# Kernel optimization log

Hardware: AMD Instinct MI355X
Metric: run time of the kernel (lower is better)

## Reference

```python
import jax, jax.numpy as jnp
import numpy as np

D_MODEL = 1024
N_HEADS = 16
D_HEAD = D_MODEL // N_HEADS
D_FF = 4096
B, S = 4, 1024
EPS = 1e-12


def layer_norm(x, gamma, beta):
    # Faithful to the torch module: unbiased std (ddof=1) and division by (std + eps).
    mean = jnp.mean(x, axis=-1, keepdims=True)
    var = jnp.sum((x - mean) ** 2, axis=-1, keepdims=True) / (x.shape[-1] - 1)
    std = jnp.sqrt(var)
    return gamma * (x - mean) / (std + EPS) + beta


def setup_inputs() -> dict:
    key = jax.random.key(0)
    ks = jax.random.split(key, 10)
    sc = lambda fan_in: 1.0 / np.sqrt(fan_in)
    inp = {
        "x": jax.random.normal(ks[0], (B, S, D_MODEL), dtype=jnp.float32),
        "ln1_g": jnp.ones((D_MODEL,), jnp.float32),
        "ln1_b": jnp.zeros((D_MODEL,), jnp.float32),
        "wq": jax.random.normal(ks[1], (D_MODEL, D_MODEL), jnp.float32) * sc(D_MODEL),
        "bq": jnp.zeros((D_MODEL,), jnp.float32),
        "wk": jax.random.normal(ks[2], (D_MODEL, D_MODEL), jnp.float32) * sc(D_MODEL),
        "bk": jnp.zeros((D_MODEL,), jnp.float32),
        "wv": jax.random.normal(ks[3], (D_MODEL, D_MODEL), jnp.float32) * sc(D_MODEL),
        "bv": jnp.zeros((D_MODEL,), jnp.float32),
        "ln2_g": jnp.ones((D_MODEL,), jnp.float32),
        "ln2_b": jnp.zeros((D_MODEL,), jnp.float32),
        "w1": jax.random.normal(ks[4], (D_FF, D_MODEL), jnp.float32) * sc(D_MODEL),
        "b1": jnp.zeros((D_FF,), jnp.float32),
        "w2": jax.random.normal(ks[5], (D_MODEL, D_FF), jnp.float32) * sc(D_FF),
        "b2": jnp.zeros((D_MODEL,), jnp.float32),
    }
    return inp


def reference(x, ln1_g, ln1_b, wq, bq, wk, bk, wv, bv, ln2_g, ln2_b, w1, b1, w2, b2):
    Bsz, Sq, D = x.shape
    residual = x
    h = layer_norm(x, ln1_g, ln1_b)
    # QKV projections (no output projection in the original module)
    q = (h @ wq.T + bq).reshape(Bsz, Sq, N_HEADS, D_HEAD)
    k = (h @ wk.T + bk).reshape(Bsz, Sq, N_HEADS, D_HEAD)
    v = (h @ wv.T + bv).reshape(Bsz, Sq, N_HEADS, D_HEAD)
    scores = jnp.einsum("bqhd,bkhd->bhqk", q, k) / np.sqrt(D_HEAD)
    attn = jax.nn.softmax(scores, axis=-1)  # [B, H, S, S]
    ctx = jnp.einsum("bhqk,bkhd->bqhd", attn, v).reshape(Bsz, Sq, D)
    out = ctx + residual
    residual = out
    h2 = layer_norm(out, ln2_g, ln2_b)
    # 1x1 conv FFN == per-token MLP with ReLU (dropout inactive at eval)
    ff = jax.nn.relu(h2 @ w1.T + b1) @ w2.T + b2
    out = ff + residual
    # torch returns attn flattened head-major: [H*B, S, S]
    attn_ret = jnp.transpose(attn, (1, 0, 2, 3)).reshape(N_HEADS * Bsz, Sq, Sq)
    return out, attn_ret
```

## Files before the change

kernel.cpp:

```cpp
#include <hip/hip_runtime.h>
#include <cstdint>
#include <cstddef>

#define SEQ 1024
#define DM 1024
#define DF 4096
#define NH 16
#define DH 64
#define BSZ 4
#define NTOK (BSZ*SEQ)
#define QKVSZ ((long)NTOK*DM)

typedef short s16x8 __attribute__((ext_vector_type(8)));
typedef float f32x4 __attribute__((ext_vector_type(4)));

__device__ __forceinline__ unsigned short f2bf(float f) {
  union { float f; unsigned u; } c; c.f = f;
  unsigned u = c.u;
  return (unsigned short)((u + 0x7fffu + ((u >> 16) & 1u)) >> 16);
}
__device__ __forceinline__ float bf2f(unsigned short b) {
  union { unsigned u; float f; } c; c.u = ((unsigned)b) << 16; return c.f;
}

__device__ __forceinline__ void gll16(const void* g, void* l) {
  __builtin_amdgcn_global_load_lds(
      (__attribute__((address_space(1))) void*)(g),
      (__attribute__((address_space(3))) void*)(l), 16, 0, 0);
}

template<int BM, int BN, int WM, int WN, int EPI>
__launch_bounds__(256)
__global__ void gemm_k(const unsigned short* __restrict__ A,
                       const unsigned short* __restrict__ W,
                       const float* __restrict__ bias,
                       void* __restrict__ outp,
                       const float* __restrict__ resid,
                       int nB, int K, int aRow, int wRow, int oRow,
                       float scale) {
  constexpr int BK = 32;
  __shared__ unsigned short At[BM*BK];
  __shared__ unsigned short Wt[BN*BK];
  const int tid = threadIdx.x;
  const int mb = (int)blockIdx.x / nB, nb = (int)blockIdx.x % nB;
  const long aBase = (long)mb*BM*aRow;
  const long wBase = (long)nb*BN*wRow;
  const int wave = tid >> 6, lane = tid & 63;
  const int quad = lane >> 4, l16 = lane & 15;
  constexpr int WGN = BN / WN;
  const int wm = (wave / WGN) * WM, wn = (wave % WGN) * WN;
  constexpr int MT = WM/16, NT = WN/16;
  f32x4 acc[MT][NT] = {};
  const int srow = tid >> 2, skof = (tid & 3) * 8;

  for (int k0 = 0; k0 < K; k0 += BK) {
#pragma unroll
    for (int r = 0; r < BM; r += 64)
      gll16(A + aBase + (long)(r + srow)*aRow + k0 + skof, &At[(r + srow)*BK + skof]);
#pragma unroll
    for (int r = 0; r < BN; r += 64)
      gll16(W + wBase + (long)(r + srow)*wRow + k0 + skof, &Wt[(r + srow)*BK + skof]);
    __syncthreads();
    s16x8 af[MT];
#pragma unroll
    for (int mt = 0; mt < MT; ++mt)
      af[mt] = *(const s16x8*)&At[(wm + mt*16 + l16)*BK + quad*8];
#pragma unroll
    for (int nt = 0; nt < NT; ++nt) {
      s16x8 bfr = *(const s16x8*)&Wt[(wn + nt*16 + l16)*BK + quad*8];
#pragma unroll
      for (int mt = 0; mt < MT; ++mt)
        acc[mt][nt] = __builtin_amdgcn_mfma_f32_16x16x32_bf16(af[mt], bfr, acc[mt][nt], 0, 0, 0);
    }
    __syncthreads();
  }

#pragma unroll
  for (int mt = 0; mt < MT; ++mt) {
#pragma unroll
    for (int nt = 0; nt < NT; ++nt) {
      const int gn = nb*BN + wn + nt*16 + l16;
      const float bv = bias ? bias[gn] : 0.f;
#pragma unroll
      for (int r = 0; r < 4; ++r) {
        const int gm = mb*BM + wm + mt*16 + quad*4 + r;
        float v = acc[mt][nt][r] + bv;
        if (EPI == 1) {
          ((unsigned short*)outp)[(long)gm*oRow + gn] = f2bf(v > 0.f ? v : 0.f);
        } else if (EPI == 3) {
          const long o = (long)gm*oRow + gn;
          ((float*)outp)[o] = v + resid[o];
        } else if (EPI == 5) {
          unsigned short* base = (unsigned short*)outp;
          const int reg = gn >> 10, cn = gn & 1023;
          if (reg == 0) {
            base[(long)gm*DM + cn] = f2bf(v * scale);
          } else if (reg == 1) {
            base[QKVSZ + (long)gm*DM + cn] = f2bf(v);
          } else {
            const int bb = gm >> 10, s = gm & 1023;
            base[2*QKVSZ + (long)bb*DM*SEQ + (long)cn*SEQ + s] = f2bf(v);
          }
        }
      }
    }
  }
}

__launch_bounds__(256)
__global__ void ln_k(const float* __restrict__ x, const float* __restrict__ g,
                     const float* __restrict__ bta, unsigned short* __restrict__ out) {
  const int row = blockIdx.x, t = threadIdx.x;
  const float4 v = ((const float4*)(x + (long)row*DM))[t];
  __shared__ float red[4];
  float s = v.x + v.y + v.z + v.w;
#pragma unroll
  for (int o = 32; o; o >>= 1) s += __shfl_down(s, o);
  if ((t & 63) == 0) red[t >> 6] = s;
  __syncthreads();
  const float mean = (red[0] + red[1] + red[2] + red[3]) * (1.f/1024.f);
  __syncthreads();
  const float dx = v.x - mean, dy = v.y - mean, dz = v.z - mean, dw = v.w - mean;
  float sq = dx*dx + dy*dy + dz*dz + dw*dw;
#pragma unroll
  for (int o = 32; o; o >>= 1) sq += __shfl_down(sq, o);
  if ((t & 63) == 0) red[t >> 6] = sq;
  __syncthreads();
  const float var = (red[0] + red[1] + red[2] + red[3]) * (1.f/1023.f);
  const float inv = 1.f / (sqrtf(var) + 1e-12f);
  const float4 gv = ((const float4*)g)[t];
  const float4 bv = ((const float4*)bta)[t];
  ushort4 o4;
  o4.x = f2bf(gv.x * dx * inv + bv.x);
  o4.y = f2bf(gv.y * dy * inv + bv.y);
  o4.z = f2bf(gv.z * dz * inv + bv.z);
  o4.w = f2bf(gv.w * dw * inv + bv.w);
  ((ushort4*)(out + (long)row*DM))[t] = o4;
}

#define R_WQ  262144L
#define R_WK  524288L
#define R_WV  786432L
#define R_W1  1835008L
#define R_W2  2883584L
#define CVT_BLOCKS 11265
__launch_bounds__(256)
__global__ void cvt5_k(const float* __restrict__ wq, const float* __restrict__ wk,
                       const float* __restrict__ wv, const float* __restrict__ w1,
                       const float* __restrict__ w2,
                       const float* __restrict__ bq, const float* __restrict__ bk,
                       const float* __restrict__ bvv,
                       unsigned short* __restrict__ wqkvb,
                       unsigned short* __restrict__ w1b,
                       unsigned short* __restrict__ w2b,
                       float* __restrict__ bcat) {
  const long blk = blockIdx.x;
  if (blk == CVT_BLOCKS - 1) {
    for (int j = threadIdx.x; j < 3072; j += 256)
      bcat[j] = j < 1024 ? bq[j] : (j < 2048 ? bk[j - 1024] : bvv[j - 2048]);
    return;
  }
  long i = blk*256 + threadIdx.x;
  const float* s; unsigned short* d;
  if (i < R_WQ)       { s = wq; d = wqkvb;              }
  else if (i < R_WK)  { s = wk; d = wqkvb + 1048576; i -= R_WQ; }
  else if (i < R_WV)  { s = wv; d = wqkvb + 2097152; i -= R_WK; }
  else if (i < R_W1)  { s = w1; d = w1b;             i -= R_WV; }
  else                { s = w2; d = w2b;             i -= R_W1; }
  const float4 v = ((const float4*)s)[i];
  ushort4 o; o.x = f2bf(v.x); o.y = f2bf(v.y); o.z = f2bf(v.z); o.w = f2bf(v.w);
  ((ushort4*)d)[i] = o;
}

#define LDP 1032
__launch_bounds__(256)
__global__ void attn_k(const unsigned short* __restrict__ Q,
                       const unsigned short* __restrict__ Kb,
                       const unsigned short* __restrict__ vt,
                       const float* __restrict__ xres,
                       float* __restrict__ attn_f,
                       float* __restrict__ out1) {
  const int b = blockIdx.y, h = blockIdx.z;
  const int q0 = blockIdx.x * 16;
  const int wave = threadIdx.x >> 6, lane = threadIdx.x & 63;
  const int quad = lane >> 4, l16 = lane & 15;
  __shared__ unsigned short PL[16 * LDP];
  __shared__ float red[4][16];

  const unsigned short* Qb = Q + (long)b*SEQ*DM + h*DH;
  const unsigned short* Kh = Kb + (long)b*SEQ*DM + h*DH;
  s16x8 af[2];
#pragma unroll
  for (int ks = 0; ks < 2; ++ks)
    af[ks] = *(const s16x8*)&Qb[(long)(q0 + l16)*DM + ks*32 + quad*8];
  f32x4 acc[16];
#pragma unroll
  for (int nt = 0; nt < 16; ++nt) acc[nt] = (f32x4){0.f, 0.f, 0.f, 0.f};
  for (int nt = 0; nt < 16; ++nt) {
    const int kc = wave*256 + nt*16 + l16;
#pragma unroll
    for (int ks = 0; ks < 2; ++ks) {
      const s16x8 bfr = *(const s16x8*)&Kh[(long)kc*DM + ks*32 + quad*8];
      acc[nt] = __builtin_amdgcn_mfma_f32_16x16x32_bf16(af[ks], bfr, acc[nt], 0, 0, 0);
    }
  }

  float rmax[4];
#pragma unroll
  for (int r = 0; r < 4; ++r) {
    float m = -3e38f;
#pragma unroll
    for (int nt = 0; nt < 16; ++nt) m = fmaxf(m, acc[nt][r]);
#pragma unroll
    for (int o = 1; o < 16; o <<= 1) m = fmaxf(m, __shfl_xor(m, o));
    rmax[r] = m;
  }
  if (l16 == 0) {
#pragma unroll
    for (int r = 0; r < 4; ++r) red[wave][quad*4 + r] = rmax[r];
  }
  __syncthreads();
#pragma unroll
  for (int r = 0; r < 4; ++r)
    rmax[r] = fmaxf(fmaxf(red[0][quad*4+r], red[1][quad*4+r]),
                    fmaxf(red[2][quad*4+r], red[3][quad*4+r]));
  __syncthreads();
#pragma unroll
  for (int r = 0; r < 4; ++r) {
    float s = 0.f;
#pragma unroll
    for (int nt = 0; nt < 16; ++nt) {
      const float e = __expf(acc[nt][r] - rmax[r]);
      acc[nt][r] = e; s += e;
    }
#pragma unroll
    for (int o = 1; o < 16; o <<= 1) s += __shfl_xor(s, o);
    if (l16 == 0) red[wave][quad*4 + r] = s;
  }
  __syncthreads();

#pragma unroll
  for (int r = 0; r < 4; ++r) {
    const float tot = red[0][quad*4+r] + red[1][quad*4+r] + red[2][quad*4+r] + red[3][quad*4+r];
    const float inv = 1.f / tot;
    unsigned short* prow = &PL[(quad*4 + r)*LDP + wave*256 + l16];
#pragma unroll
    for (int nt = 0; nt < 16; ++nt)
      prow[nt*16] = f2bf(acc[nt][r] * inv);
  }
  __syncthreads();

  {
    const long obase = (long)(h*BSZ + b)*SEQ*SEQ + (long)q0*SEQ;
    const int col = threadIdx.x * 4;
#pragma unroll
    for (int row = 0; row < 16; ++row) {
      const ushort4 pv = *(const ushort4*)&PL[row*LDP + col];
      float4 o;
      o.x = bf2f(pv.x); o.y = bf2f(pv.y); o.z = bf2f(pv.z); o.w = bf2f(pv.w);
      ((float4*)(attn_f + obase + (long)row*SEQ))[threadIdx.x] = o;
    }
  }

  f32x4 c = (f32x4){0.f, 0.f, 0.f, 0.f};
  const unsigned short* Vh = vt + (long)b*DM*SEQ + (long)(h*DH + wave*16 + l16)*SEQ;
#pragma unroll 4
  for (int k0 = 0; k0 < 32; ++k0) {
    const s16x8 a  = *(const s16x8*)&PL[l16*LDP + k0*32 + quad*8];
    const s16x8 bf = *(const s16x8*)&Vh[k0*32 + quad*8];
    c = __builtin_amdgcn_mfma_f32_16x16x32_bf16(a, bf, c, 0, 0, 0);
  }

#pragma unroll
  for (int r = 0; r < 4; ++r) {
    const int gq = q0 + quad*4 + r;
    const int col = h*DH + wave*16 + l16;
    const long idx = (long)b*SEQ*DM + (long)gq*DM + col;
    out1[idx] = c[r] + xres[idx];
  }
}

extern "C" void kernel_launch(void* const* d_in, const int* in_sizes, int n_in,
                              void* d_out, int out_size, void* d_ws, size_t ws_size,
                              hipStream_t stream) {
  const float* x    = (const float*)d_in[0];
  const float* ln1g = (const float*)d_in[1];
  const float* ln1b = (const float*)d_in[2];
  const float* wq   = (const float*)d_in[3];
  const float* bq   = (const float*)d_in[4];
  const float* wk   = (const float*)d_in[5];
  const float* bk   = (const float*)d_in[6];
  const float* wv   = (const float*)d_in[7];
  const float* bv   = (const float*)d_in[8];
  const float* ln2g = (const float*)d_in[9];
  const float* ln2b = (const float*)d_in[10];
  const float* w1   = (const float*)d_in[11];
  const float* b1   = (const float*)d_in[12];
  const float* w2   = (const float*)d_in[13];
  const float* b2   = (const float*)d_in[14];
  float* out    = (float*)d_out;
  float* attn_f = out + (long)NTOK*DM;

  uint8_t* p = (uint8_t*)d_ws;
  auto alloc = [&](size_t bytes) {
    uint8_t* r = p; p += (bytes + 255) & ~(size_t)255; return r;
  };
  unsigned short* hbuf  = (unsigned short*)alloc((size_t)NTOK*DM*2);
  unsigned short* qkv   = (unsigned short*)alloc((size_t)3*NTOK*DM*2);
  unsigned short* h2    = (unsigned short*)alloc((size_t)NTOK*DM*2);
  unsigned short* f1    = (unsigned short*)alloc((size_t)NTOK*DF*2);
  float*          out1  = (float*)alloc((size_t)NTOK*DM*4);
  unsigned short* wqkvb = (unsigned short*)alloc((size_t)3*DM*DM*2);
  unsigned short* w1b   = (unsigned short*)alloc((size_t)DF*DM*2);
  unsigned short* w2b   = (unsigned short*)alloc((size_t)DM*DF*2);
  float*          bcat  = (float*)alloc((size_t)3*DM*4);

  cvt5_k<<<CVT_BLOCKS, 256, 0, stream>>>(wq, wk, wv, w1, w2, bq, bk, bv,
                                         wqkvb, w1b, w2b, bcat);
  ln_k<<<NTOK, 256, 0, stream>>>(x, ln1g, ln1b, hbuf);

  gemm_k<128,128,64,64,5><<<dim3((NTOK/128)*(3*DM/128)), 256, 0, stream>>>(
      hbuf, wqkvb, bcat, qkv, nullptr, 3*DM/128, DM, DM, DM, DM, 0.125f);

  attn_k<<<dim3(SEQ/16, BSZ, NH), 256, 0, stream>>>(
      qkv, qkv + QKVSZ, qkv + 2*QKVSZ, x, attn_f, out1);

  ln_k<<<NTOK, 256, 0, stream>>>(out1, ln2g, ln2b, h2);

  gemm_k<128,128,64,64,1><<<dim3((NTOK/128)*(DF/128)), 256, 0, stream>>>(
      h2, w1b, b1, f1, nullptr, DF/128, DM, DM, DM, DF, 1.f);

  gemm_k<128,128,64,64,3><<<dim3((NTOK/128)*(DM/128)), 256, 0, stream>>>(
      f1, w2b, b2, out, out1, DM/128, DF, DF, DF, DM, 1.f);
}
```

Measured before the change: 684.4 us.

## Split-K the FFN2 GEMM, vectorize V-transpose stores, fuse attn output writes

The final FFN GEMM (K=4096, only 256 blocks) is split into two K halves over a second grid dimension, writing fp32 partials that a new combine kernel sums with bias and residual. This raises block count and parallelism but adds 32 MB of partial traffic and an extra launch. Separately, the QKV epilogue writes the transposed V region as 4-wide vector stores, and the attention kernel writes fp32 probabilities directly from registers instead of re-reading them from LDS. The P·V loop also now uses four independent accumulators to break the MFMA dependency chain.

```diff
diff --git a/kernel.cpp b/kernel.cpp
--- a/kernel.cpp
+++ b/kernel.cpp
@@ -42,6 +42,11 @@
   __shared__ unsigned short At[BM*BK];
   __shared__ unsigned short Wt[BN*BK];
   const int tid = threadIdx.x;
+  const int kz = blockIdx.y;
+  A += (long)kz * K;
+  W += (long)kz * K;
+  float* outF = (float*)outp;
+  if (EPI == 7) outF += (long)kz * ((long)(gridDim.x / nB) * BM) * oRow;
   const int mb = (int)blockIdx.x / nB, nb = (int)blockIdx.x % nB;
   const long aBase = (long)mb*BM*aRow;
   const long wBase = (long)nb*BN*wRow;
@@ -81,30 +86,62 @@
     for (int nt = 0; nt < NT; ++nt) {
       const int gn = nb*BN + wn + nt*16 + l16;
       const float bv = bias ? bias[gn] : 0.f;
-#pragma unroll
-      for (int r = 0; r < 4; ++r) {
-        const int gm = mb*BM + wm + mt*16 + quad*4 + r;
-        float v = acc[mt][nt][r] + bv;
-        if (EPI == 1) {
-          ((unsigned short*)outp)[(long)gm*oRow + gn] = f2bf(v > 0.f ? v : 0.f);
-        } else if (EPI == 3) {
-          const long o = (long)gm*oRow + gn;
-          ((float*)outp)[o] = v + resid[o];
-        } else if (EPI == 5) {
-          unsigned short* base = (unsigned short*)outp;
-          const int reg = gn >> 10, cn = gn & 1023;
-          if (reg == 0) {
-            base[(long)gm*DM + cn] = f2bf(v * scale);
-          } else if (reg == 1) {
-            base[QKVSZ + (long)gm*DM + cn] = f2bf(v);
-          } else {
-            const int bb = gm >> 10, s = gm & 1023;
-            base[2*QKVSZ + (long)bb*DM*SEQ + (long)cn*SEQ + s] = f2bf(v);
+      if (EPI == 5) {
+        unsigned short* base = (unsigned short*)outp;
+        const int reg = gn >> 10, cn = gn & 1023;
+        if (reg == 2) {
+          const int gm0 = mb*BM + wm + mt*16 + quad*4;
+          const int bb = gm0 >> 10, s0 = gm0 & 1023;
+          ushort4 o4;
+          o4.x = f2bf(acc[mt][nt][0] + bv);
+          o4.y = f2bf(acc[mt][nt][1] + bv);
+          o4.z = f2bf(acc[mt][nt][2] + bv);
+          o4.w = f2bf(acc[mt][nt][3] + bv);
+          *(ushort4*)&base[2*QKVSZ + (long)bb*DM*SEQ + (long)cn*SEQ + s0] = o4;
+        } else {
+#pragma unroll
+          for (int r = 0; r < 4; ++r) {
+            const int gm = mb*BM + wm + mt*16 + quad*4 + r;
+            const float v = acc[mt][nt][r] + bv;
+            if (reg == 0) base[(long)gm*DM + cn] = f2bf(v * scale);
+            else          base[QKVSZ + (long)gm*DM + cn] = f2bf(v);
+          }
+        }
+      } else {
+#pragma unroll
+        for (int r = 0; r < 4; ++r) {
+          const int gm = mb*BM + wm + mt*16 + quad*4 + r;
+          float v = acc[mt][nt][r] + bv;
+          if (EPI == 1) {
+            ((unsigned short*)outp)[(long)gm*oRow + gn] = f2bf(v > 0.f ? v : 0.f);
+          } else if (EPI == 3) {
+            const long o = (long)gm*oRow + gn;
+            ((float*)outp)[o] = v + resid[o];
+          } else if (EPI == 7) {
+            outF[(long)gm*oRow + gn] = v;
           }
         }
       }
     }
   }
+}
+
+__launch_bounds__(256)
+__global__ void comb_k(const float* __restrict__ p,
+                       const float* __restrict__ b2,
+                       const float* __restrict__ out1,
+                       float* __restrict__ out) {
+  const int i = blockIdx.x * 256 + threadIdx.x;
+  const float4 a = ((const float4*)p)[i];
+  const float4 b = ((const float4*)(p + (long)NTOK*DM))[i];
+  const float4 bb = ((const float4*)b2)[i & (DM/4 - 1)];
+  const float4 r = ((const float4*)out1)[i];
+  float4 o;
+  o.x = a.x + b.x + bb.x + r.x;
+  o.y = a.y + b.y + bb.y + r.y;
+  o.z = a.z + b.z + bb.z + r.z;
+  o.w = a.w + b.w + bb.w + r.w;
+  ((float4*)out)[i] = o;
 }
 
 __launch_bounds__(256)
@@ -239,37 +276,31 @@
   }
   __syncthreads();
 
+  const long obase = (long)(h*BSZ + b)*SEQ*SEQ + (long)q0*SEQ;
 #pragma unroll
   for (int r = 0; r < 4; ++r) {
     const float tot = red[0][quad*4+r] + red[1][quad*4+r] + red[2][quad*4+r] + red[3][quad*4+r];
     const float inv = 1.f / tot;
     unsigned short* prow = &PL[(quad*4 + r)*LDP + wave*256 + l16];
-#pragma unroll
-    for (int nt = 0; nt < 16; ++nt)
-      prow[nt*16] = f2bf(acc[nt][r] * inv);
-  }
-  __syncthreads();
-
-  {
-    const long obase = (long)(h*BSZ + b)*SEQ*SEQ + (long)q0*SEQ;
-    const int col = threadIdx.x * 4;
-#pragma unroll
-    for (int row = 0; row < 16; ++row) {
-      const ushort4 pv = *(const ushort4*)&PL[row*LDP + col];
-      float4 o;
-      o.x = bf2f(pv.x); o.y = bf2f(pv.y); o.z = bf2f(pv.z); o.w = bf2f(pv.w);
-      ((float4*)(attn_f + obase + (long)row*SEQ))[threadIdx.x] = o;
-    }
-  }
-
-  f32x4 c = (f32x4){0.f, 0.f, 0.f, 0.f};
+    float* arow = attn_f + obase + (long)(quad*4 + r)*SEQ + wave*256 + l16;
+#pragma unroll
+    for (int nt = 0; nt < 16; ++nt) {
+      const float pv_ = acc[nt][r] * inv;
+      prow[nt*16] = f2bf(pv_);
+      arow[nt*16] = pv_;
+    }
+  }
+  __syncthreads();
+
+  f32x4 cc[4] = {};
   const unsigned short* Vh = vt + (long)b*DM*SEQ + (long)(h*DH + wave*16 + l16)*SEQ;
-#pragma unroll 4
+#pragma unroll
   for (int k0 = 0; k0 < 32; ++k0) {
     const s16x8 a  = *(const s16x8*)&PL[l16*LDP + k0*32 + quad*8];
     const s16x8 bf = *(const s16x8*)&Vh[k0*32 + quad*8];
-    c = __builtin_amdgcn_mfma_f32_16x16x32_bf16(a, bf, c, 0, 0, 0);
-  }
+    cc[k0 & 3] = __builtin_amdgcn_mfma_f32_16x16x32_bf16(a, bf, cc[k0 & 3], 0, 0, 0);
+  }
+  const f32x4 c = (cc[0] + cc[1]) + (cc[2] + cc[3]);
 
 #pragma unroll
   for (int r = 0; r < 4; ++r) {
@@ -314,6 +345,7 @@
   unsigned short* w1b   = (unsigned short*)alloc((size_t)DF*DM*2);
   unsigned short* w2b   = (unsigned short*)alloc((size_t)DM*DF*2);
   float*          bcat  = (float*)alloc((size_t)3*DM*4);
+  float*          part  = (float*)alloc((size_t)2*NTOK*DM*4);
 
   cvt5_k<<<CVT_BLOCKS, 256, 0, stream>>>(wq, wk, wv, w1, w2, bq, bk, bv,
                                          wqkvb, w1b, w2b, bcat);
@@ -330,6 +362,7 @@
   gemm_k<128,128,64,64,1><<<dim3((NTOK/128)*(DF/128)), 256, 0, stream>>>(
       h2, w1b, b1, f1, nullptr, DF/128, DM, DM, DM, DF, 1.f);
 
-  gemm_k<128,128,64,64,3><<<dim3((NTOK/128)*(DM/128)), 256, 0, stream>>>(
-      f1, w2b, b2, out, out1, DM/128, DF, DF, DF, DM, 1.f);
-}
+  gemm_k<128,128,64,64,7><<<dim3((NTOK/128)*(DM/128), 2), 256, 0, stream>>>(
+      f1, w2b, nullptr, part, nullptr, DM/128, DF/2, DF, DF, DM, 1.f);
+  comb_k<<<(NTOK*DM)/1024, 256, 0, stream>>>(part, b2, out1, out);
+}
```

Result: faster. 649.4 us (-5.1%).
